# Optimization experiments

Hardware: AMD Instinct MI355X
Metric: run time of the kernel (lower is better)

## Reference

```python
import jax, jax.numpy as jnp
import numpy as np
import math

B, S, D, H, NH = 2, 2048, 1024, 16, 8
DK = D // H


def setup_inputs() -> dict:
    key = jax.random.key(0)
    ks = jax.random.split(key, 10)
    s = 1.0 / math.sqrt(D)
    return {
        "x": jax.random.normal(ks[0], (B, S, D), jnp.float32),
        "Wq": jax.random.normal(ks[1], (D, D), jnp.float32) * s,
        "bq": jnp.zeros((D,), jnp.float32),
        "Wk": jax.random.normal(ks[2], (D, D), jnp.float32) * s,
        "bk": jnp.zeros((D,), jnp.float32),
        "Wv": jax.random.normal(ks[3], (D, D), jnp.float32) * s,
        "bv": jnp.zeros((D,), jnp.float32),
        "Wo": jax.random.normal(ks[4], (D, D), jnp.float32) * s,
        "bo": jnp.zeros((D,), jnp.float32),
        "R": jax.random.normal(ks[5], (NH, DK), jnp.float32),
    }


def reference(x, Wq, bq, Wk, bk, Wv, bv, Wo, bo, R):
    b, s, _ = x.shape
    # projections -> [B, S, H, DK]
    Q = (x @ Wq + bq).reshape(b, s, H, DK)
    K = (x @ Wk + bk).reshape(b, s, H, DK)
    V = (x @ Wv + bv).reshape(b, s, H, DK)
    # LSH buckets: argmax over random projections -> [B, S, H] -> [B, H, S]
    qb = jnp.argmax(jnp.einsum('bshd,nd->bshn', Q, R), axis=-1).transpose(0, 2, 1)
    kb = jnp.argmax(jnp.einsum('bshd,nd->bshn', K, R), axis=-1).transpose(0, 2, 1)
    # bucket-equality mask [B, H, S, S]
    mask = qb[:, :, :, None] == kb[:, :, None, :]
    # attention: [B, H, S, S]
    scores = jnp.einsum('bihd,bjhd->bhij', Q, K) / jnp.sqrt(jnp.float32(DK))
    scores = jnp.where(mask, scores, -jnp.inf)
    probs = jax.nn.softmax(scores, axis=-1)
    out = jnp.einsum('bhij,bjhd->bihd', probs, V).reshape(b, s, D)
    return out @ Wo + bo
```

## Files before the change

### kernel.cpp

```cpp
#include <hip/hip_runtime.h>
#include <hip/hip_bf16.h>


typedef __bf16 bf16;
typedef __bf16 bf16x8 __attribute__((ext_vector_type(8)));
typedef __bf16 bf16x4 __attribute__((ext_vector_type(4)));
typedef float f32x4 __attribute__((ext_vector_type(4)));

#define DEV static __device__ __forceinline__

DEV f32x4 zero4() { f32x4 z; z[0]=0.f; z[1]=0.f; z[2]=0.f; z[3]=0.f; return z; }

DEV f32x4 mfma_bf16(bf16x8 a, bf16x8 b, f32x4 c) {
  return __builtin_amdgcn_mfma_f32_16x16x32_bf16(a, b, c, 0, 0, 0);
}

DEV void load_lds16(const bf16* g, bf16* l) {
  __builtin_amdgcn_global_load_lds(
      (const __attribute__((address_space(1))) void*)g,
      (__attribute__((address_space(3))) void*)l, 16, 0, 0);
}

DEV void split3(float f, bf16& h, bf16& m, bf16& l) {
  h = (bf16)f;
  float rm = f - (float)h;
  m = (bf16)rm;
  l = (bf16)(rm - (float)m);
}

#define B_  2
#define S_  2048
#define D_  1024
#define H_  16
#define NH_ 8
#define DK_ 64
#define M_  4096
#define QPAD 2560
#define NQT  40

__global__ __launch_bounds__(256) void k_prep(
    const float* __restrict__ Wq, const float* __restrict__ Wk,
    const float* __restrict__ Wv, const float* __restrict__ Wo,
    const float* __restrict__ x, const float* __restrict__ bq,
    const float* __restrict__ bk, const float* __restrict__ R,
    bf16* __restrict__ Wtq, bf16* __restrict__ Wtk,
    bf16* __restrict__ Wtv, bf16* __restrict__ Wto,
    bf16* __restrict__ xh, bf16* __restrict__ Pth, bf16* __restrict__ Ptm,
    bf16* __restrict__ Ptl, float* __restrict__ bt) {
  __shared__ float tile[64][65];
  __shared__ float Rl[512];
  const int t = threadIdx.x;
  const int z = blockIdx.z;
  if (z < 4) {
    const float* W = z == 0 ? Wq : z == 1 ? Wk : z == 2 ? Wv : Wo;
    bf16* Wt = z == 0 ? Wtq : z == 1 ? Wtk : z == 2 ? Wtv : Wto;
    int k0 = blockIdx.x * 64, n0 = blockIdx.y * 64;
    int c = t & 63, r4 = t >> 6;
#pragma unroll
    for (int i = 0; i < 16; i++) {
      int r = r4 * 16 + i;
      tile[r][c] = W[(k0 + r) * D_ + n0 + c];
    }
    __syncthreads();
#pragma unroll
    for (int i = 0; i < 16; i++) {
      int r = r4 * 16 + i;
      Wt[(n0 + r) * D_ + k0 + c] = (bf16)tile[c][r];
    }
  } else if (z == 4) {
    int bid = blockIdx.y * 16 + blockIdx.x;
    int base = bid * 16384 + t * 4;
#pragma unroll 4
    for (int it = 0; it < 16; it++) {
      int i = base + it * 1024;
      f32x4 v = *(const f32x4*)(x + i);
      bf16x4 o;
#pragma unroll
      for (int j = 0; j < 4; j++) o[j] = (bf16)v[j];
      *(bf16x4*)(xh + i) = o;
    }
  } else {
    int bid = blockIdx.y * 16 + blockIdx.x;
    if (bid >= 64) return;
    Rl[t] = R[t];
    Rl[t + 256] = R[t + 256];
    __syncthreads();
    const int d0 = bid * 16;
    const int sel = t >> 7, hn = t & 127, h = hn >> 3, n = hn & 7;
    const float* W = sel ? Wk : Wq;
    const float* Rr = &Rl[n * 64];
    bf16x8 vh[2], vm[2], vl[2];
#pragma unroll
    for (int dl = 0; dl < 16; dl++) {
      const float* wr = W + (d0 + dl) * D_ + h * 64;
      float acc = 0.f;
#pragma unroll
      for (int k = 0; k < 64; k += 4) {
        f32x4 wv = *(const f32x4*)(wr + k);
        acc += (wv[0] * Rr[k] + wv[1] * Rr[k + 1]) +
               (wv[2] * Rr[k + 2] + wv[3] * Rr[k + 3]);
      }
      bf16 hh, mm, ll;
      split3(acc, hh, mm, ll);
      vh[dl >> 3][dl & 7] = hh;
      vm[dl >> 3][dl & 7] = mm;
      vl[dl >> 3][dl & 7] = ll;
    }
    *(bf16x8*)&Pth[t * D_ + d0] = vh[0];
    *(bf16x8*)&Pth[t * D_ + d0 + 8] = vh[1];
    *(bf16x8*)&Ptm[t * D_ + d0] = vm[0];
    *(bf16x8*)&Ptm[t * D_ + d0 + 8] = vm[1];
    *(bf16x8*)&Ptl[t * D_ + d0] = vl[0];
    *(bf16x8*)&Ptl[t * D_ + d0 + 8] = vl[1];
    if (bid == 0) {
      const float* bb = sel ? bk : bq;
      float acc = 0.f;
#pragma unroll 8
      for (int k = 0; k < 64; k++) acc += bb[h * 64 + k] * Rr[k];
      bt[t] = acc;
    }
  }
}

__global__ __launch_bounds__(256) void k_main(
    const float* __restrict__ x, const bf16* __restrict__ xh,
    const bf16* __restrict__ Wtq, const bf16* __restrict__ Wtk,
    const bf16* __restrict__ Wtv, const float* __restrict__ bq,
    const float* __restrict__ bk, const float* __restrict__ bv,
    const bf16* __restrict__ Pth, const bf16* __restrict__ Ptm,
    const bf16* __restrict__ Ptl,
    bf16* __restrict__ Qb, bf16* __restrict__ Kb, bf16* __restrict__ Vb,
    float* __restrict__ Lpart) {
  __shared__ __align__(16) bf16 SA[3][2048];
  __shared__ __align__(16) bf16 SB[3][2048];
  const int t = threadIdx.x;
  const int lane = t & 63, w = t >> 6;
  const int lm = lane & 15, qd = lane >> 4;
  const int srow = lane >> 2, sseg = lane & 3;

  if (blockIdx.y < 24) {
    if (blockIdx.x >= 32) return;
    bf16* Al = &SA[0][0];
    bf16* Bl = &SB[0][0];
    const int m0 = blockIdx.x * 128;
    const int mat = blockIdx.y >> 3;
    const int n0 = (blockIdx.y & 7) * 128;
    const bf16* Bt = mat == 0 ? Wtq : (mat == 1 ? Wtk : Wtv);
    const float* bias = mat == 0 ? bq : (mat == 1 ? bk : bv);
    bf16* out = mat == 0 ? Qb : (mat == 1 ? Kb : Vb);
    const int wm = w >> 1, wn = w & 1;

    f32x4 acc[4][4];
#pragma unroll
    for (int i = 0; i < 4; i++)
#pragma unroll
      for (int j = 0; j < 4; j++) acc[i][j] = zero4();

    for (int k0 = 0; k0 < D_; k0 += 32) {
      __syncthreads();
      load_lds16(&xh[(m0 + w * 16 + srow) * D_ + k0 + sseg * 8],
                 &Al[(w * 16) * 32]);
      load_lds16(&xh[(m0 + 64 + w * 16 + srow) * D_ + k0 + sseg * 8],
                 &Al[(64 + w * 16) * 32]);
      load_lds16(&Bt[(n0 + w * 16 + srow) * D_ + k0 + sseg * 8],
                 &Bl[(w * 16) * 32]);
      load_lds16(&Bt[(n0 + 64 + w * 16 + srow) * D_ + k0 + sseg * 8],
                 &Bl[(64 + w * 16) * 32]);
      __syncthreads();
      bf16x8 af[4], bfr[4];
#pragma unroll
      for (int i = 0; i < 4; i++)
        af[i] = *(const bf16x8*)&Al[(wm * 64 + i * 16 + lm) * 32 + qd * 8];
#pragma unroll
      for (int j = 0; j < 4; j++)
        bfr[j] = *(const bf16x8*)&Bl[(wn * 64 + j * 16 + lm) * 32 + qd * 8];
#pragma unroll
      for (int i = 0; i < 4; i++)
#pragma unroll
        for (int j = 0; j < 4; j++)
          acc[i][j] = mfma_bf16(af[i], bfr[j], acc[i][j]);
    }
#pragma unroll
    for (int j = 0; j < 4; j++) {
      int n = n0 + wn * 64 + j * 16 + lm;
      float bv2 = bias[n];
#pragma unroll
      for (int i = 0; i < 4; i++) {
        int mbase = m0 + wm * 64 + i * 16 + qd * 4;
#pragma unroll
        for (int r = 0; r < 4; r++) {
          int m = mbase + r;
          int bb = m >> 11, s = m & 2047, hh = n >> 6, d = n & 63;
          out[((bb * H_ + hh) * S_ + s) * DK_ + d] = (bf16)(acc[i][j][r] + bv2);
        }
      }
    }
  } else {
    const int yy = blockIdx.y - 24;
    const int chunk = yy >> 2;
    const int m0 = blockIdx.x * 64, n0 = (yy & 3) * 64;
    f32x4 acc[4];
#pragma unroll
    for (int nb = 0; nb < 4; nb++) acc[nb] = zero4();
    const int xrow = t >> 2, xc8 = (t & 3) * 8;
    const int kbeg = chunk * 256, kend = kbeg + 256;

    for (int k0 = kbeg; k0 < kend; k0 += 32) {
      __syncthreads();
      f32x4 xa = *(const f32x4*)&x[(m0 + xrow) * D_ + k0 + xc8];
      f32x4 xb2 = *(const f32x4*)&x[(m0 + xrow) * D_ + k0 + xc8 + 4];
      bf16x8 vh, vm, vl;
#pragma unroll
      for (int j = 0; j < 4; j++) {
        bf16 hh, mm, ll;
        split3(xa[j], hh, mm, ll);
        vh[j] = hh; vm[j] = mm; vl[j] = ll;
        split3(xb2[j], hh, mm, ll);
        vh[4 + j] = hh; vm[4 + j] = mm; vl[4 + j] = ll;
      }
      *(bf16x8*)&SA[0][xrow * 32 + xc8] = vh;
      *(bf16x8*)&SA[1][xrow * 32 + xc8] = vm;
      *(bf16x8*)&SA[2][xrow * 32 + xc8] = vl;
      load_lds16(&Pth[(n0 + w * 16 + srow) * D_ + k0 + sseg * 8],
                 &SB[0][(w * 16) * 32]);
      load_lds16(&Ptm[(n0 + w * 16 + srow) * D_ + k0 + sseg * 8],
                 &SB[1][(w * 16) * 32]);
      load_lds16(&Ptl[(n0 + w * 16 + srow) * D_ + k0 + sseg * 8],
                 &SB[2][(w * 16) * 32]);
      __syncthreads();
      bf16x8 af[3], bfr[3][4];
#pragma unroll
      for (int i3 = 0; i3 < 3; i3++) {
        af[i3] = *(const bf16x8*)&SA[i3][(w * 16 + lm) * 32 + qd * 8];
#pragma unroll
        for (int nb = 0; nb < 4; nb++)
          bfr[i3][nb] = *(const bf16x8*)&SB[i3][(nb * 16 + lm) * 32 + qd * 8];
      }
#pragma unroll
      for (int nb = 0; nb < 4; nb++) {
        f32x4 a = acc[nb];
        a = mfma_bf16(af[0], bfr[0][nb], a);
        a = mfma_bf16(af[0], bfr[1][nb], a);
        a = mfma_bf16(af[1], bfr[0][nb], a);
        a = mfma_bf16(af[0], bfr[2][nb], a);
        a = mfma_bf16(af[2], bfr[0][nb], a);
        a = mfma_bf16(af[1], bfr[1][nb], a);
        acc[nb] = a;
      }
    }
    float* Lp = Lpart + chunk * (M_ * 256);
#pragma unroll
    for (int nb = 0; nb < 4; nb++)
#pragma unroll
      for (int r = 0; r < 4; r++)
        Lp[(m0 + w * 16 + qd * 4 + r) * 256 + n0 + nb * 16 + lm] = acc[nb][r];
  }
}

__global__ __launch_bounds__(256) void k_amax(const float* __restrict__ Lpart,
                                              const float* __restrict__ bt,
                                              int* __restrict__ qb,
                                              int* __restrict__ kb) {
  const int t = threadIdx.x;
  const int row = blockIdx.x * 16 + (t >> 4);
  const int c0 = (t & 15) * 16;
  const float* L0 = Lpart + row * 256 + c0;
  float v[16];
#pragma unroll
  for (int c4 = 0; c4 < 16; c4 += 4) {
    f32x4 p0 = *(const f32x4*)(L0 + c4);
    f32x4 p1 = *(const f32x4*)(L0 + 1 * M_ * 256 + c4);
    f32x4 p2 = *(const f32x4*)(L0 + 2 * M_ * 256 + c4);
    f32x4 p3 = *(const f32x4*)(L0 + 3 * M_ * 256 + c4);
    f32x4 bv = *(const f32x4*)(bt + c0 + c4);
#pragma unroll
    for (int j = 0; j < 4; j++)
      v[c4 + j] = (((p0[j] + p1[j]) + p2[j]) + p3[j]) + bv[j];
  }
  const int bb = row >> 11, s = row & 2047;
#pragma unroll
  for (int g2 = 0; g2 < 2; g2++) {
    float best = v[g2 * 8];
    int bi = 0;
#pragma unroll
    for (int n = 1; n < 8; n++)
      if (v[g2 * 8 + n] > best) { best = v[g2 * 8 + n]; bi = n; }
    int g = (c0 >> 3) + g2;
    int sel = g >> 4, head = g & 15;
    (sel ? kb : qb)[(bb * H_ + head) * S_ + s] = bi;
  }
}

__global__ __launch_bounds__(256) void k_sort(const int* __restrict__ qb,
                                              const int* __restrict__ kb,
                                              int* __restrict__ qidx,
                                              int* __restrict__ kidx,
                                              int2* __restrict__ meta) {
  __shared__ int cnt[8][257];
  __shared__ int bst[2][9];
  __shared__ int tot[2][8];
  const int bh = blockIdx.x;
  const int t = threadIdx.x;
  const int lane = t & 63, w = t >> 6;
  for (int which = 0; which < 2; which++) {
    const int* src = (which ? kb : qb) + bh * S_;
    int* dst = (which ? kidx : qidx) + bh * QPAD;
    for (int i = t; i < QPAD; i += 256) dst[i] = -1;
    int vals[8];
    int lc[8] = {0, 0, 0, 0, 0, 0, 0, 0};
#pragma unroll
    for (int j = 0; j < 8; j++) { int b = src[t * 8 + j]; vals[j] = b; lc[b]++; }
#pragma unroll
    for (int b = 0; b < 8; b++) cnt[b][t] = lc[b];
    __syncthreads();
    for (int bb = w; bb < 8; bb += 4) {
      int carry = 0;
      for (int round = 0; round < 4; round++) {
        int v = cnt[bb][round * 64 + lane];
        int inc = v;
#pragma unroll
        for (int off = 1; off < 64; off <<= 1) {
          int u = __shfl_up(inc, off);
          if (lane >= off) inc += u;
        }
        cnt[bb][round * 64 + lane] = carry + inc - v;
        carry += __shfl(inc, 63);
      }
      if (lane == 0) tot[which][bb] = carry;
    }
    __syncthreads();
    if (t == 0) {
      int pos = 0;
      for (int b = 0; b < 8; b++) {
        bst[which][b] = pos;
        pos += (tot[which][b] + 63) & ~63;
      }
      bst[which][8] = pos;
    }
    __syncthreads();
    int run2[8] = {0, 0, 0, 0, 0, 0, 0, 0};
#pragma unroll
    for (int j = 0; j < 8; j++) {
      int b = vals[j];
      int pos = bst[which][b] + cnt[b][t] + run2[b]++;
      dst[pos] = t * 8 + j;
    }
    __syncthreads();
  }
  if (t == 0) {
    for (int tt = 0; tt < NQT; tt++) meta[bh * NQT + tt] = make_int2(0, 0);
    for (int b = 0; b < 8; b++) {
      int t0 = bst[0][b] >> 6;
      int nt = ((tot[0][b] + 63) & ~63) >> 6;
      int ks = bst[1][b];
      int nkt = (tot[1][b] + 63) >> 6;
      for (int tt = t0; tt < t0 + nt; tt++)
        meta[bh * NQT + tt] = make_int2(ks, nkt);
    }
  }
}

__global__ __launch_bounds__(256) void k_attn(const bf16* __restrict__ Q,
                                              const bf16* __restrict__ K,
                                              const bf16* __restrict__ V,
                                              const int* __restrict__ qidx,
                                              const int* __restrict__ kidx,
                                              const int2* __restrict__ meta,
                                              bf16* __restrict__ O) {
  constexpr int LDK = 72;
  __shared__ bf16 Kl[64 * LDK];
  __shared__ bf16 Vl[64 * LDK];
  __shared__ bf16 Pl[64 * LDK];
  __shared__ int kbl[64];
  __shared__ int qsl[64];
  const int t = threadIdx.x;
  const int qt = blockIdx.x, h = blockIdx.y, b = blockIdx.z;
  const int lane = t & 63, w = t >> 6;
  const int lm = lane & 15, qd = lane >> 4;
  const int bh = b * H_ + h;

  const int2 mt = meta[bh * NQT + qt];
  const int kstart = mt.x, nkt = mt.y;

  if (t < 64) qsl[t] = qidx[bh * QPAD + qt * 64 + t];
  __syncthreads();

  if (nkt == 0) {
#pragma unroll
    for (int r = 0; r < 4; r++) {
      int qs = qsl[w * 16 + qd * 4 + r];
      if (qs >= 0)
#pragma unroll
        for (int nb = 0; nb < 4; nb++)
          O[((b * S_ + qs) * H_ + h) * DK_ + nb * 16 + lm] = (bf16)0.f;
    }
    return;
  }

  int qrow = qsl[w * 16 + lm];
  const bf16* Qp = Q + (bh * S_ + (qrow < 0 ? 0 : qrow)) * DK_;
  bf16x8 qf0 = *(const bf16x8*)(Qp + qd * 8);
  bf16x8 qf1 = *(const bf16x8*)(Qp + 32 + qd * 8);

  f32x4 oacc[4];
  float mrun[4], lrun[4];
#pragma unroll
  for (int nb = 0; nb < 4; nb++) oacc[nb] = zero4();
#pragma unroll
  for (int r = 0; r < 4; r++) { mrun[r] = -1e30f; lrun[r] = 0.f; }

  const bf16* Kbase = K + bh * S_ * DK_;
  const bf16* Vbase = V + bh * S_ * DK_;
  const int* kix = kidx + bh * QPAD + kstart;

  for (int kt = 0; kt < nkt; kt++) {
    const int kt0 = kt * 64;
    __syncthreads();
    if (t < 64) kbl[t] = kix[kt0 + t];
#pragma unroll
    for (int ss = 0; ss < 2; ss++) {
      int seg = t + ss * 256;
      int row = seg >> 3, sg = seg & 7;
      int ki = kix[kt0 + row]; ki = ki < 0 ? 0 : ki;
      *(bf16x8*)&Kl[row * LDK + sg * 8] =
          *(const bf16x8*)&Kbase[ki * DK_ + sg * 8];
    }
#pragma unroll
    for (int ss = 0; ss < 2; ss++) {
      int seg = t + ss * 256;
      int vrow = seg & 63, vsg = seg >> 6;
      int ki = kix[kt0 + vrow]; ki = ki < 0 ? 0 : ki;
      bf16x8 v8 = *(const bf16x8*)&Vbase[ki * DK_ + vsg * 8];
#pragma unroll
      for (int j = 0; j < 8; j++) Vl[(vsg * 8 + j) * LDK + vrow] = v8[j];
    }
    __syncthreads();

    f32x4 sc[4];
#pragma unroll
    for (int nb = 0; nb < 4; nb++) {
      bf16x8 kf0 = *(const bf16x8*)&Kl[(nb * 16 + lm) * LDK + qd * 8];
      bf16x8 kf1 = *(const bf16x8*)&Kl[(nb * 16 + lm) * LDK + 32 + qd * 8];
      f32x4 z = zero4();
      z = mfma_bf16(qf0, kf0, z);
      z = mfma_bf16(qf1, kf1, z);
      sc[nb] = z;
    }
#pragma unroll
    for (int nb = 0; nb < 4; nb++) {
      bool valid = kbl[nb * 16 + lm] >= 0;
#pragma unroll
      for (int r = 0; r < 4; r++)
        sc[nb][r] = valid ? sc[nb][r] * 0.125f : -1e30f;
    }
    float mnew[4], alpha[4], rs[4];
#pragma unroll
    for (int r = 0; r < 4; r++) {
      float tm = fmaxf(fmaxf(sc[0][r], sc[1][r]), fmaxf(sc[2][r], sc[3][r]));
      tm = fmaxf(tm, __shfl_xor(tm, 1));
      tm = fmaxf(tm, __shfl_xor(tm, 2));
      tm = fmaxf(tm, __shfl_xor(tm, 4));
      tm = fmaxf(tm, __shfl_xor(tm, 8));
      mnew[r] = fmaxf(mrun[r], tm);
      alpha[r] = __expf(mrun[r] - mnew[r]);
      mrun[r] = mnew[r];
      rs[r] = 0.f;
    }
#pragma unroll
    for (int nb = 0; nb < 4; nb++)
#pragma unroll
      for (int r = 0; r < 4; r++) {
        float p = (sc[nb][r] > -1e29f) ? __expf(sc[nb][r] - mnew[r]) : 0.f;
        sc[nb][r] = p;
        rs[r] += p;
      }
#pragma unroll
    for (int r = 0; r < 4; r++) {
      float s = rs[r];
      s += __shfl_xor(s, 1);
      s += __shfl_xor(s, 2);
      s += __shfl_xor(s, 4);
      s += __shfl_xor(s, 8);
      lrun[r] = lrun[r] * alpha[r] + s;
    }
#pragma unroll
    for (int nb = 0; nb < 4; nb++)
#pragma unroll
      for (int r = 0; r < 4; r++) oacc[nb][r] *= alpha[r];
#pragma unroll
    for (int nb = 0; nb < 4; nb++)
#pragma unroll
      for (int r = 0; r < 4; r++)
        Pl[(w * 16 + qd * 4 + r) * LDK + nb * 16 + lm] = (bf16)sc[nb][r];
    __syncthreads();
    bf16x8 pa0 = *(const bf16x8*)&Pl[(w * 16 + lm) * LDK + qd * 8];
    bf16x8 pa1 = *(const bf16x8*)&Pl[(w * 16 + lm) * LDK + 32 + qd * 8];
#pragma unroll
    for (int nb = 0; nb < 4; nb++) {
      bf16x8 vf0 = *(const bf16x8*)&Vl[(nb * 16 + lm) * LDK + qd * 8];
      bf16x8 vf1 = *(const bf16x8*)&Vl[(nb * 16 + lm) * LDK + 32 + qd * 8];
      oacc[nb] = mfma_bf16(pa0, vf0, oacc[nb]);
      oacc[nb] = mfma_bf16(pa1, vf1, oacc[nb]);
    }
  }
#pragma unroll
  for (int r = 0; r < 4; r++) {
    int qs = qsl[w * 16 + qd * 4 + r];
    if (qs < 0) continue;
    float l = lrun[r];
    float inv = (l > 0.f) ? 1.f / l : 0.f;
#pragma unroll
    for (int nb = 0; nb < 4; nb++)
      O[((b * S_ + qs) * H_ + h) * DK_ + nb * 16 + lm] = (bf16)(oacc[nb][r] * inv);
  }
}

__global__ __launch_bounds__(256) void k_gout(const bf16* __restrict__ A,
                                              const bf16* __restrict__ Bt,
                                              const float* __restrict__ bias,
                                              float* __restrict__ out) {
  __shared__ __align__(16) bf16 Al[64 * 32];
  __shared__ __align__(16) bf16 Bl[128 * 32];
  const int t = threadIdx.x;
  const int lane = t & 63, w = t >> 6;
  const int lm = lane & 15, qd = lane >> 4;
  const int srow = lane >> 2, sseg = lane & 3;
  const int m0 = blockIdx.x * 64, n0 = blockIdx.y * 128;
  const int wm = w >> 1, wn = w & 1;

  f32x4 acc[2][4];
#pragma unroll
  for (int i = 0; i < 2; i++)
#pragma unroll
    for (int j = 0; j < 4; j++) acc[i][j] = zero4();

  for (int k0 = 0; k0 < D_; k0 += 32) {
    __syncthreads();
    load_lds16(&A[(m0 + w * 16 + srow) * D_ + k0 + sseg * 8],
               &Al[(w * 16) * 32]);
    load_lds16(&Bt[(n0 + w * 16 + srow) * D_ + k0 + sseg * 8],
               &Bl[(w * 16) * 32]);
    load_lds16(&Bt[(n0 + 64 + w * 16 + srow) * D_ + k0 + sseg * 8],
               &Bl[(64 + w * 16) * 32]);
    __syncthreads();
    bf16x8 af[2], bfr[4];
#pragma unroll
    for (int i = 0; i < 2; i++)
      af[i] = *(const bf16x8*)&Al[(wm * 32 + i * 16 + lm) * 32 + qd * 8];
#pragma unroll
    for (int j = 0; j < 4; j++)
      bfr[j] = *(const bf16x8*)&Bl[(wn * 64 + j * 16 + lm) * 32 + qd * 8];
#pragma unroll
    for (int i = 0; i < 2; i++)
#pragma unroll
      for (int j = 0; j < 4; j++) acc[i][j] = mfma_bf16(af[i], bfr[j], acc[i][j]);
  }
#pragma unroll
  for (int j = 0; j < 4; j++) {
    int n = n0 + wn * 64 + j * 16 + lm;
    float bv = bias[n];
#pragma unroll
    for (int i = 0; i < 2; i++) {
      int mbase = m0 + wm * 32 + i * 16 + qd * 4;
#pragma unroll
      for (int r = 0; r < 4; r++)
        out[(mbase + r) * D_ + n] = acc[i][j][r] + bv;
    }
  }
}

extern "C" void kernel_launch(void* const* d_in, const int* in_sizes, int n_in,
                              void* d_out, int out_size, void* d_ws, size_t ws_size,
                              hipStream_t stream) {
  (void)in_sizes; (void)n_in; (void)out_size; (void)ws_size;
  const float* x  = (const float*)d_in[0];
  const float* Wq = (const float*)d_in[1];
  const float* bq = (const float*)d_in[2];
  const float* Wk = (const float*)d_in[3];
  const float* bk = (const float*)d_in[4];
  const float* Wv = (const float*)d_in[5];
  const float* bv = (const float*)d_in[6];
  const float* Wo = (const float*)d_in[7];
  const float* bo = (const float*)d_in[8];
  const float* R  = (const float*)d_in[9];

  char* ws = (char*)d_ws;
  bf16*  xh   = (bf16*)(ws + 0);
  bf16*  Qb   = (bf16*)(ws + 8388608);
  bf16*  Kb   = (bf16*)(ws + 16777216);
  bf16*  Vb   = (bf16*)(ws + 25165824);
  bf16*  Ob   = (bf16*)(ws + 33554432);
  bf16*  Wtq  = (bf16*)(ws + 41943040);
  bf16*  Wtk  = (bf16*)(ws + 44040192);
  bf16*  Wtv  = (bf16*)(ws + 46137344);
  bf16*  Wto  = (bf16*)(ws + 48234496);
  int*   qbuf = (int*)(ws + 51380224);
  int*   kbuf = (int*)(ws + 51642368);
  float* bt   = (float*)(ws + 51904512);
  bf16*  Pth  = (bf16*)(ws + 51905536);
  bf16*  Ptm  = (bf16*)(ws + 52429824);
  bf16*  Ptl  = (bf16*)(ws + 52954112);
  int*   qidxp= (int*)(ws + 53478400);
  int*   kidxp= (int*)(ws + 53806080);
  int2*  meta = (int2*)(ws + 54133760);
  float* Lpart= (float*)(ws + 67108864);

  k_prep<<<dim3(16, 16, 6), dim3(256), 0, stream>>>(
      Wq, Wk, Wv, Wo, x, bq, bk, R, Wtq, Wtk, Wtv, Wto, xh, Pth, Ptm, Ptl, bt);

  k_main<<<dim3(64, 40), dim3(256), 0, stream>>>(
      x, xh, Wtq, Wtk, Wtv, bq, bk, bv, Pth, Ptm, Ptl, Qb, Kb, Vb, Lpart);

  k_amax<<<dim3(256), dim3(256), 0, stream>>>(Lpart, bt, qbuf, kbuf);

  k_sort<<<dim3(32), dim3(256), 0, stream>>>(qbuf, kbuf, qidxp, kidxp, meta);

  k_attn<<<dim3(NQT, H_, B_), dim3(256), 0, stream>>>(Qb, Kb, Vb, qidxp, kidxp,
                                                      meta, Ob);

  k_gout<<<dim3(64, 8), dim3(256), 0, stream>>>(Ob, Wto, bo, (float*)d_out);
}
```

Measured before the change: 220.5 us.

## Double-buffer K/V tiles in attention and fold score scale into Q

Measured after the change: 217.7 us. No clear change (-1.3%).

```diff
diff --git a/kernel.cpp b/kernel.cpp
--- a/kernel.cpp
+++ b/kernel.cpp
@@ -148,6 +148,7 @@
     const bf16* Bt = mat == 0 ? Wtq : (mat == 1 ? Wtk : Wtv);
     const float* bias = mat == 0 ? bq : (mat == 1 ? bk : bv);
     bf16* out = mat == 0 ? Qb : (mat == 1 ? Kb : Vb);
+    const float osc = mat == 0 ? 0.125f : 1.f;
     const int wm = w >> 1, wn = w & 1;
 
     f32x4 acc[4][4];
@@ -191,7 +192,8 @@
         for (int r = 0; r < 4; r++) {
           int m = mbase + r;
           int bb = m >> 11, s = m & 2047, hh = n >> 6, d = n & 63;
-          out[((bb * H_ + hh) * S_ + s) * DK_ + d] = (bf16)(acc[i][j][r] + bv2);
+          out[((bb * H_ + hh) * S_ + s) * DK_ + d] =
+              (bf16)((acc[i][j][r] + bv2) * osc);
         }
       }
     }
@@ -209,6 +211,12 @@
       __syncthreads();
       f32x4 xa = *(const f32x4*)&x[(m0 + xrow) * D_ + k0 + xc8];
       f32x4 xb2 = *(const f32x4*)&x[(m0 + xrow) * D_ + k0 + xc8 + 4];
+      load_lds16(&Pth[(n0 + w * 16 + srow) * D_ + k0 + sseg * 8],
+                 &SB[0][(w * 16) * 32]);
+      load_lds16(&Ptm[(n0 + w * 16 + srow) * D_ + k0 + sseg * 8],
+                 &SB[1][(w * 16) * 32]);
+      load_lds16(&Ptl[(n0 + w * 16 + srow) * D_ + k0 + sseg * 8],
+                 &SB[2][(w * 16) * 32]);
       bf16x8 vh, vm, vl;
 #pragma unroll
       for (int j = 0; j < 4; j++) {
@@ -221,12 +229,6 @@
       *(bf16x8*)&SA[0][xrow * 32 + xc8] = vh;
       *(bf16x8*)&SA[1][xrow * 32 + xc8] = vm;
       *(bf16x8*)&SA[2][xrow * 32 + xc8] = vl;
-      load_lds16(&Pth[(n0 + w * 16 + srow) * D_ + k0 + sseg * 8],
-                 &SB[0][(w * 16) * 32]);
-      load_lds16(&Ptm[(n0 + w * 16 + srow) * D_ + k0 + sseg * 8],
-                 &SB[1][(w * 16) * 32]);
-      load_lds16(&Ptl[(n0 + w * 16 + srow) * D_ + k0 + sseg * 8],
-                 &SB[2][(w * 16) * 32]);
       __syncthreads();
       bf16x8 af[3], bfr[3][4];
 #pragma unroll
@@ -368,10 +370,10 @@
                                               const int2* __restrict__ meta,
                                               bf16* __restrict__ O) {
   constexpr int LDK = 72;
-  __shared__ bf16 Kl[64 * LDK];
-  __shared__ bf16 Vl[64 * LDK];
+  __shared__ bf16 Kl[2][64 * LDK];
+  __shared__ bf16 Vl[2][64 * LDK];
   __shared__ bf16 Pl[64 * LDK];
-  __shared__ int kbl[64];
+  __shared__ int kbl[2][64];
   __shared__ int qsl[64];
   const int t = threadIdx.x;
   const int qt = blockIdx.x, h = blockIdx.y, b = blockIdx.z;
@@ -413,34 +415,52 @@
   const bf16* Vbase = V + bh * S_ * DK_;
   const int* kix = kidx + bh * QPAD + kstart;
 
+  const int krow0 = t >> 3, ksg = t & 7;
+  const int krow1 = (t + 256) >> 3;
+  const int vrow0 = t & 63, vsg0 = t >> 6;
+  const int vsg1 = vsg0 + 4;
+
+  {
+    if (t < 64) kbl[0][t] = kix[t];
+    int ki0 = kix[krow0]; ki0 = ki0 < 0 ? 0 : ki0;
+    int ki1 = kix[krow1]; ki1 = ki1 < 0 ? 0 : ki1;
+    *(bf16x8*)&Kl[0][krow0 * LDK + ksg * 8] =
+        *(const bf16x8*)&Kbase[ki0 * DK_ + ksg * 8];
+    *(bf16x8*)&Kl[0][krow1 * LDK + ksg * 8] =
+        *(const bf16x8*)&Kbase[ki1 * DK_ + ksg * 8];
+    int kv = kix[vrow0]; kv = kv < 0 ? 0 : kv;
+    bf16x8 v0 = *(const bf16x8*)&Vbase[kv * DK_ + vsg0 * 8];
+    bf16x8 v1 = *(const bf16x8*)&Vbase[kv * DK_ + vsg1 * 8];
+#pragma unroll
+    for (int j = 0; j < 8; j++) {
+      Vl[0][(vsg0 * 8 + j) * LDK + vrow0] = v0[j];
+      Vl[0][(vsg1 * 8 + j) * LDK + vrow0] = v1[j];
+    }
+  }
+  __syncthreads();
+
   for (int kt = 0; kt < nkt; kt++) {
-    const int kt0 = kt * 64;
-    __syncthreads();
-    if (t < 64) kbl[t] = kix[kt0 + t];
-#pragma unroll
-    for (int ss = 0; ss < 2; ss++) {
-      int seg = t + ss * 256;
-      int row = seg >> 3, sg = seg & 7;
-      int ki = kix[kt0 + row]; ki = ki < 0 ? 0 : ki;
-      *(bf16x8*)&Kl[row * LDK + sg * 8] =
-          *(const bf16x8*)&Kbase[ki * DK_ + sg * 8];
-    }
-#pragma unroll
-    for (int ss = 0; ss < 2; ss++) {
-      int seg = t + ss * 256;
-      int vrow = seg & 63, vsg = seg >> 6;
-      int ki = kix[kt0 + vrow]; ki = ki < 0 ? 0 : ki;
-      bf16x8 v8 = *(const bf16x8*)&Vbase[ki * DK_ + vsg * 8];
-#pragma unroll
-      for (int j = 0; j < 8; j++) Vl[(vsg * 8 + j) * LDK + vrow] = v8[j];
-    }
-    __syncthreads();
+    const int cur = kt & 1, nxt = cur ^ 1;
+    const bool more = (kt + 1 < nkt);
+    bf16x8 kn0, kn1, vn0, vn1;
+    int kbn = 0;
+    if (more) {
+      const int kt1 = (kt + 1) * 64;
+      if (t < 64) kbn = kix[kt1 + t];
+      int ki0 = kix[kt1 + krow0]; ki0 = ki0 < 0 ? 0 : ki0;
+      int ki1 = kix[kt1 + krow1]; ki1 = ki1 < 0 ? 0 : ki1;
+      kn0 = *(const bf16x8*)&Kbase[ki0 * DK_ + ksg * 8];
+      kn1 = *(const bf16x8*)&Kbase[ki1 * DK_ + ksg * 8];
+      int kv = kix[kt1 + vrow0]; kv = kv < 0 ? 0 : kv;
+      vn0 = *(const bf16x8*)&Vbase[kv * DK_ + vsg0 * 8];
+      vn1 = *(const bf16x8*)&Vbase[kv * DK_ + vsg1 * 8];
+    }
 
     f32x4 sc[4];
 #pragma unroll
     for (int nb = 0; nb < 4; nb++) {
-      bf16x8 kf0 = *(const bf16x8*)&Kl[(nb * 16 + lm) * LDK + qd * 8];
-      bf16x8 kf1 = *(const bf16x8*)&Kl[(nb * 16 + lm) * LDK + 32 + qd * 8];
+      bf16x8 kf0 = *(const bf16x8*)&Kl[cur][(nb * 16 + lm) * LDK + qd * 8];
+      bf16x8 kf1 = *(const bf16x8*)&Kl[cur][(nb * 16 + lm) * LDK + 32 + qd * 8];
       f32x4 z = zero4();
       z = mfma_bf16(qf0, kf0, z);
       z = mfma_bf16(qf1, kf1, z);
@@ -448,10 +468,10 @@
     }
 #pragma unroll
     for (int nb = 0; nb < 4; nb++) {
-      bool valid = kbl[nb * 16 + lm] >= 0;
+      bool valid = kbl[cur][nb * 16 + lm] >= 0;
 #pragma unroll
       for (int r = 0; r < 4; r++)
-        sc[nb][r] = valid ? sc[nb][r] * 0.125f : -1e30f;
+        sc[nb][r] = valid ? sc[nb][r] : -1e30f;
     }
     float mnew[4], alpha[4], rs[4];
 #pragma unroll
@@ -492,15 +512,25 @@
 #pragma unroll
       for (int r = 0; r < 4; r++)
         Pl[(w * 16 + qd * 4 + r) * LDK + nb * 16 + lm] = (bf16)sc[nb][r];
-    __syncthreads();
     bf16x8 pa0 = *(const bf16x8*)&Pl[(w * 16 + lm) * LDK + qd * 8];
     bf16x8 pa1 = *(const bf16x8*)&Pl[(w * 16 + lm) * LDK + 32 + qd * 8];
 #pragma unroll
     for (int nb = 0; nb < 4; nb++) {
-      bf16x8 vf0 = *(const bf16x8*)&Vl[(nb * 16 + lm) * LDK + qd * 8];
-      bf16x8 vf1 = *(const bf16x8*)&Vl[(nb * 16 + lm) * LDK + 32 + qd * 8];
+      bf16x8 vf0 = *(const bf16x8*)&Vl[cur][(nb * 16 + lm) * LDK + qd * 8];
+      bf16x8 vf1 = *(const bf16x8*)&Vl[cur][(nb * 16 + lm) * LDK + 32 + qd * 8];
       oacc[nb] = mfma_bf16(pa0, vf0, oacc[nb]);
       oacc[nb] = mfma_bf16(pa1, vf1, oacc[nb]);
+    }
+    if (more) {
+      if (t < 64) kbl[nxt][t] = kbn;
+      *(bf16x8*)&Kl[nxt][krow0 * LDK + ksg * 8] = kn0;
+      *(bf16x8*)&Kl[nxt][krow1 * LDK + ksg * 8] = kn1;
+#pragma unroll
+      for (int j = 0; j < 8; j++) {
+        Vl[nxt][(vsg0 * 8 + j) * LDK + vrow0] = vn0[j];
+        Vl[nxt][(vsg1 * 8 + j) * LDK + vrow0] = vn1[j];
+      }
+      __syncthreads();
     }
   }
 #pragma unroll
@@ -606,7 +636,8 @@
   float* Lpart= (float*)(ws + 67108864);
 
   k_prep<<<dim3(16, 16, 6), dim3(256), 0, stream>>>(
-      Wq, Wk, Wv, Wo, x, bq, bk, R, Wtq, Wtk, Wtv, Wto, xh, Pth, Ptm, Ptl, bt);
+      Wq, Wk, Wv, Wo, x, bq, bk, R, Wtq, Wtk, Wtv, Wto, xh,
+      Pth, Ptm, Ptl, bt);
 
   k_main<<<dim3(64, 40), dim3(256), 0, stream>>>(
       x, xh, Wtq, Wtk, Wtv, bq, bk, bv, Pth, Ptm, Ptl, Qb, Kb, Vb, Lpart);
```
